# Performance work log

Hardware: AMD Instinct MI355X
Metric: run time of the kernel (lower is better)

Reference implementation:

```python
import jax, jax.numpy as jnp
import numpy as np

KH, KW = 5, 5  # filter_size


def setup_inputs() -> dict:
    key = jax.random.key(0)
    k1, k2 = jax.random.split(key)
    n, c, t, h, w = 1, 3, 25, 128, 128
    filter_prod = KH * KW  # 25
    up_sq = 16
    x = jax.random.normal(k1, (n, c, t, h, w), dtype=jnp.float32)
    filters = jax.random.uniform(k2, (n, filter_prod, up_sq, t, h, w), dtype=jnp.float32)
    return {"x": x, "filters": filters}


def reference(x, filters):
    # x: (n, 3, t, h, w); filters: (n, kh*kw, up_sq, t, h, w)
    n, c, t, h, w = x.shape
    up_sq = filters.shape[2]
    ph, pw = KH // 2, KW // 2
    # The torch module's 25 one-hot grouped conv2d calls are exactly im2col:
    # patch k = a*KW + b is x shifted by (a-ph, b-pw) with zero padding.
    xp = jnp.pad(x, ((0, 0), (0, 0), (0, 0), (ph, ph), (pw, pw)))
    patches = jnp.stack(
        [xp[:, :, :, a:a + h, b:b + w] for a in range(KH) for b in range(KW)],
        axis=-1,
    )  # (n, 3, t, h, w, kh*kw)
    out = jnp.einsum('ncthwk,nkuthw->ncuthw', patches, filters)
    # (n, 3, up_sq, t, h, w) -> (n, 3*up_sq, t, h, w)
    return out.reshape(n, c * up_sq, t, h, w)
```

## Files before the change

### kernel.cpp

```cpp
#include <hip/hip_runtime.h>


#define T_ 25
#define H_ 128
#define W_ 128
#define C_ 3
#define U_ 16
#define KH_ 5
#define KW_ 5
#define HW_ (H_ * W_)
#define THW_ (T_ * HW_)

__global__ __launch_bounds__(256) void duf_kernel(
    const float* __restrict__ x,
    const float* __restrict__ filt,
    float* __restrict__ out)
{
    const int p = blockIdx.x * blockDim.x + threadIdx.x;
    const int t = p / HW_;
    const int rem = p - t * HW_;
    const int h = rem / W_;
    const int w = rem - h * W_;

    float acc[C_][U_];
#pragma unroll
    for (int c = 0; c < C_; ++c)
#pragma unroll
        for (int u = 0; u < U_; ++u) acc[c][u] = 0.f;

    const float* xb = x + (size_t)t * HW_ + (size_t)h * W_ + w;

#pragma unroll
    for (int a = 0; a < KH_; ++a) {
        const int hh = h + a - 2;
        const bool hok = (hh >= 0) & (hh < H_);
#pragma unroll
        for (int b = 0; b < KW_; ++b) {
            const int ww = w + b - 2;
            const bool ok = hok & (ww >= 0) & (ww < W_);
            const int k = a * KW_ + b;
            const int off = (a - 2) * W_ + (b - 2);
            float p0 = 0.f, p1 = 0.f, p2 = 0.f;
            if (ok) {
                p0 = xb[0 * T_ * HW_ + off];
                p1 = xb[1 * T_ * HW_ + off];
                p2 = xb[2 * T_ * HW_ + off];
            }
            const float* fp = filt + (size_t)k * U_ * THW_ + p;
#pragma unroll
            for (int u = 0; u < U_; ++u) {
                const float f = fp[(size_t)u * THW_];
                acc[0][u] += p0 * f;
                acc[1][u] += p1 * f;
                acc[2][u] += p2 * f;
            }
        }
    }

#pragma unroll
    for (int c = 0; c < C_; ++c)
#pragma unroll
        for (int u = 0; u < U_; ++u)
            out[(size_t)(c * U_ + u) * THW_ + p] = acc[c][u];
}

extern "C" void kernel_launch(void* const* d_in, const int* in_sizes, int n_in,
                              void* d_out, int out_size, void* d_ws, size_t ws_size,
                              hipStream_t stream) {
    const float* x = (const float*)d_in[0];
    const float* filt = (const float*)d_in[1];
    float* out = (float*)d_out;
    dim3 grid(THW_ / 256);
    dim3 block(256);
    duf_kernel<<<grid, block, 0, stream>>>(x, filt, out);
}
```

Before: 881.3 us.

## Stage input tile in LDS and vectorize filter loads and outputs with float4

Each block loads a padded 6x132 input tile for all three channels into shared memory, removing the bounds-checked global gathers. Work is redistributed so each thread handles four contiguous pixels and four up-channels, using float4 loads for filters and float4 stores for outputs. This is meant to cut load instruction count and raise effective bandwidth on the dominant filter stream. It adds a sync per block and reduces per-thread parallelism on the filter stream.

After: 854.4 us. 3.1% less time.

```diff
diff --git a/kernel.cpp b/kernel.cpp
--- a/kernel.cpp
+++ b/kernel.cpp
@@ -11,48 +11,78 @@
 #define HW_ (H_ * W_)
 #define THW_ (T_ * HW_)
 
+#define BLOCK_PIX 256
+#define LROWS 6
+#define LCOLS 132
+
 __global__ __launch_bounds__(256) void duf_kernel(
     const float* __restrict__ x,
     const float* __restrict__ filt,
     float* __restrict__ out)
 {
-    const int p = blockIdx.x * blockDim.x + threadIdx.x;
-    const int t = p / HW_;
-    const int rem = p - t * HW_;
-    const int h = rem / W_;
-    const int w = rem - h * W_;
+    __shared__ __align__(16) float xs[C_ * LROWS * LCOLS];
 
-    float acc[C_][U_];
+    const int tid = threadIdx.x;
+    const int P0  = blockIdx.x * BLOCK_PIX;
+    const int t   = P0 / HW_;
+    const int h0  = (P0 - t * HW_) / W_;
+
+    const float* xt = x + (size_t)t * HW_;
+    for (int idx = tid; idx < C_ * LROWS * LCOLS; idx += 256) {
+        const int c   = idx / (LROWS * LCOLS);
+        const int rem = idx - c * (LROWS * LCOLS);
+        const int r   = rem / LCOLS;
+        const int col = rem - r * LCOLS;
+        const int gh  = h0 - 2 + r;
+        const int gw  = col - 2;
+        float v = 0.f;
+        if ((unsigned)gh < (unsigned)H_ && (unsigned)gw < (unsigned)W_)
+            v = xt[(size_t)c * THW_ + gh * W_ + gw];
+        xs[idx] = v;
+    }
+    __syncthreads();
+
+    const int lane = tid & 63;
+    const int uq   = tid >> 6;
+    const int p0   = P0 + lane * 4;
+    const int lrow = lane >> 5;
+    const int w0   = (lane & 31) * 4;
+
+    float4 acc[C_][4];
 #pragma unroll
     for (int c = 0; c < C_; ++c)
 #pragma unroll
-        for (int u = 0; u < U_; ++u) acc[c][u] = 0.f;
+        for (int u = 0; u < 4; ++u)
+            acc[c][u] = make_float4(0.f, 0.f, 0.f, 0.f);
 
-    const float* xb = x + (size_t)t * HW_ + (size_t)h * W_ + w;
+    const float* fb = filt + (size_t)(uq * 4) * THW_ + p0;
 
+#pragma unroll 1
+    for (int a = 0; a < KH_; ++a) {
+        float xr[C_][8];
 #pragma unroll
-    for (int a = 0; a < KH_; ++a) {
-        const int hh = h + a - 2;
-        const bool hok = (hh >= 0) & (hh < H_);
+        for (int c = 0; c < C_; ++c) {
+            const float4* s =
+                (const float4*)&xs[(c * LROWS + lrow + a) * LCOLS + w0];
+            const float4 lo = s[0];
+            const float4 hi = s[1];
+            xr[c][0] = lo.x; xr[c][1] = lo.y; xr[c][2] = lo.z; xr[c][3] = lo.w;
+            xr[c][4] = hi.x; xr[c][5] = hi.y; xr[c][6] = hi.z; xr[c][7] = hi.w;
+        }
+        const float* fa = fb + (size_t)a * (KW_ * U_) * THW_;
 #pragma unroll
         for (int b = 0; b < KW_; ++b) {
-            const int ww = w + b - 2;
-            const bool ok = hok & (ww >= 0) & (ww < W_);
-            const int k = a * KW_ + b;
-            const int off = (a - 2) * W_ + (b - 2);
-            float p0 = 0.f, p1 = 0.f, p2 = 0.f;
-            if (ok) {
-                p0 = xb[0 * T_ * HW_ + off];
-                p1 = xb[1 * T_ * HW_ + off];
-                p2 = xb[2 * T_ * HW_ + off];
-            }
-            const float* fp = filt + (size_t)k * U_ * THW_ + p;
 #pragma unroll
-            for (int u = 0; u < U_; ++u) {
-                const float f = fp[(size_t)u * THW_];
-                acc[0][u] += p0 * f;
-                acc[1][u] += p1 * f;
-                acc[2][u] += p2 * f;
+            for (int u = 0; u < 4; ++u) {
+                const float4 f =
+                    *(const float4*)(fa + (size_t)(b * U_ + u) * THW_);
+#pragma unroll
+                for (int c = 0; c < C_; ++c) {
+                    acc[c][u].x += xr[c][b + 0] * f.x;
+                    acc[c][u].y += xr[c][b + 1] * f.y;
+                    acc[c][u].z += xr[c][b + 2] * f.z;
+                    acc[c][u].w += xr[c][b + 3] * f.w;
+                }
             }
         }
     }
@@ -60,8 +90,9 @@
 #pragma unroll
     for (int c = 0; c < C_; ++c)
 #pragma unroll
-        for (int u = 0; u < U_; ++u)
-            out[(size_t)(c * U_ + u) * THW_ + p] = acc[c][u];
+        for (int u = 0; u < 4; ++u)
+            *(float4*)(out + (size_t)(c * U_ + uq * 4 + u) * THW_ + p0) =
+                acc[c][u];
 }
 
 extern "C" void kernel_launch(void* const* d_in, const int* in_sizes, int n_in,
@@ -70,7 +101,7 @@
     const float* x = (const float*)d_in[0];
     const float* filt = (const float*)d_in[1];
     float* out = (float*)d_out;
-    dim3 grid(THW_ / 256);
+    dim3 grid(THW_ / BLOCK_PIX);
     dim3 block(256);
     duf_kernel<<<grid, block, 0, stream>>>(x, filt, out);
 }
```
